# Performance work log

Hardware: AMD Instinct MI355X
Metric: run time of the kernel (lower is better)

Reference implementation:

```python
import jax, jax.numpy as jnp
import numpy as np

B, S, E, H = 2, 2048, 1024, 16
D = E // H  # dim per head


def setup_inputs() -> dict:
    key = jax.random.key(0)
    ks = jax.random.split(key, 13)
    sc = 1.0 / np.sqrt(E)
    inp = {
        "query": jax.random.normal(ks[0], (B, S, E), jnp.float32),
        "key": jax.random.normal(ks[1], (B, S, E), jnp.float32),
        "value": jax.random.normal(ks[2], (B, S, E), jnp.float32),
        "mask": jax.random.randint(ks[3], (B, S, S), 0, 2, jnp.int32),
        "Wq": jax.random.normal(ks[4], (E, E), jnp.float32) * sc,
        "bq": jnp.zeros((E,), jnp.float32),
        "Wk": jax.random.normal(ks[5], (E, E), jnp.float32) * sc,
        "bk": jnp.zeros((E,), jnp.float32),
        "Wv": jax.random.normal(ks[6], (E, E), jnp.float32) * sc,
        "bv": jnp.zeros((E,), jnp.float32),
        "Wo": jax.random.normal(ks[7], (E, E), jnp.float32) * sc,
        "bo": jnp.zeros((E,), jnp.float32),
    }
    return inp


def _split_heads(x):
    # [B, S, E] -> [B, H, S, D]
    return x.reshape(B, S, H, D).transpose(0, 2, 1, 3)


def reference(query, key, value, mask, Wq, bq, Wk, bk, Wv, bv, Wo, bo):
    q = _split_heads(query @ Wq.T + bq)
    k = _split_heads(key @ Wk.T + bk)
    v = _split_heads(value @ Wv.T + bv)

    dk = k.shape[-1]
    # scores: [B, H, Sq, Sk]
    scores = jnp.einsum("bhqd,bhkd->bhqk", q / jnp.sqrt(jnp.asarray(dk, q.dtype)), k)
    # mask broadcast over heads: [B, 1, Sq, Sk]; masked positions get -1e9
    scores = jnp.where(mask[:, None, :, :] == 0, jnp.asarray(-1e9, scores.dtype), scores)
    # fp32 softmax (dropout is identity in eval mode)
    attn = jax.nn.softmax(scores.astype(jnp.float32), axis=-1).astype(q.dtype)
    out = jnp.einsum("bhqk,bhkd->bhqd", attn, v)
    out = out.transpose(0, 2, 1, 3).reshape(B, S, E)
    return out @ Wo.T + bo
```

## Files before the change

kernel.cpp:

```cpp
#include <hip/hip_runtime.h>
#include <hip/hip_bf16.h>
#include <stdint.h>


typedef __bf16 bf16x8 __attribute__((ext_vector_type(8)));
typedef __bf16 bf16x4 __attribute__((ext_vector_type(4)));
typedef float  f32x4  __attribute__((ext_vector_type(4)));
typedef unsigned int u32x4 __attribute__((ext_vector_type(4)));

#define MFMA16(a, b, c) __builtin_amdgcn_mfma_f32_16x16x32_bf16((a), (b), (c), 0, 0, 0)

#if __has_builtin(__builtin_amdgcn_exp2f)
#define EXP2(x) __builtin_amdgcn_exp2f(x)
#else
#define EXP2(x) exp2f(x)
#endif

static constexpr int kB = 2, kS = 2048, kE = 1024, kH = 16, kD = 64;
static constexpr int kM = kB * kS;
static constexpr int kMaskWordsPerRow = kS / 64;
static constexpr float kLog2e = 1.4426950408889634f;

__device__ __forceinline__ void gload_lds16(const void* g, void* l) {
  __builtin_amdgcn_global_load_lds(
      (const __attribute__((address_space(1))) unsigned int*)g,
      (__attribute__((address_space(3))) unsigned int*)l, 16, 0, 0);
}

__device__ __forceinline__ unsigned pack_bf16x2(float a, float b) {
  unsigned short lo = __builtin_bit_cast(unsigned short, (__bf16)a);
  unsigned short hi = __builtin_bit_cast(unsigned short, (__bf16)b);
  return (unsigned)lo | ((unsigned)hi << 16);
}

__global__ __launch_bounds__(256) void cvt_pack_kernel(
    const float* __restrict__ q, const float* __restrict__ k, const float* __restrict__ v,
    const float* __restrict__ wq, const float* __restrict__ wk,
    const float* __restrict__ wv, const float* __restrict__ wo,
    const int* __restrict__ mask,
    __bf16* __restrict__ qb, __bf16* __restrict__ kb, __bf16* __restrict__ vb,
    __bf16* __restrict__ wqb, __bf16* __restrict__ wkb,
    __bf16* __restrict__ wvb, __bf16* __restrict__ wob,
    unsigned long long* __restrict__ mw) {
  const int z = blockIdx.y;
  if (z == 7) {
    const int lane = threadIdx.x & 63;
    const int wid = (blockIdx.x * blockDim.x + threadIdx.x) >> 6;
    const int nwaves = (gridDim.x * blockDim.x) >> 6;
    const int nwords = kB * kS * kMaskWordsPerRow;
    for (int w = wid; w < nwords; w += nwaves) {
      int mv = mask[(size_t)w * 64 + lane];
      unsigned long long bits = __ballot(mv != 0);
      if (lane == 0) mw[w] = bits;
    }
    return;
  }
  const float* src; __bf16* dst; int n;
  switch (z) {
    case 0: src = q;  dst = qb;  n = kM * kE; break;
    case 1: src = k;  dst = kb;  n = kM * kE; break;
    case 2: src = v;  dst = vb;  n = kM * kE; break;
    case 3: src = wq; dst = wqb; n = kE * kE; break;
    case 4: src = wk; dst = wkb; n = kE * kE; break;
    case 5: src = wv; dst = wvb; n = kE * kE; break;
    default: src = wo; dst = wob; n = kE * kE; break;
  }
  const int n4 = n >> 2;
  const int stride = gridDim.x * blockDim.x;
  for (int i = blockIdx.x * blockDim.x + threadIdx.x; i < n4; i += stride) {
    float4 f = ((const float4*)src)[i];
    bf16x4 o = {(__bf16)f.x, (__bf16)f.y, (__bf16)f.z, (__bf16)f.w};
    ((bf16x4*)dst)[i] = o;
  }
}

__global__ __launch_bounds__(256) void gemm_bt(
    const __bf16* __restrict__ A0, const __bf16* __restrict__ A1, const __bf16* __restrict__ A2,
    const __bf16* __restrict__ W0, const __bf16* __restrict__ W1, const __bf16* __restrict__ W2,
    const float* __restrict__ b0, const float* __restrict__ b1, const float* __restrict__ b2,
    __bf16* __restrict__ O0, __bf16* __restrict__ O1, __bf16* __restrict__ O2) {
  const int z = blockIdx.z;
  const __bf16* A = (z == 0) ? A0 : (z == 1) ? A1 : A2;
  const __bf16* W = (z == 0) ? W0 : (z == 1) ? W1 : W2;
  const float* bias = (z == 0) ? b0 : (z == 1) ? b1 : b2;
  __bf16* OutB = (z == 0) ? O0 : (z == 1) ? O1 : O2;
  const float scale = (z == 0) ? 0.125f * kLog2e : 1.0f;

  const int n0 = blockIdx.x * 128;
  const int m0 = blockIdx.y * 128;
  const int tid = threadIdx.x;
  const int wave = tid >> 6, lane = tid & 63;
  const int g = lane >> 4, qi = lane & 15;
  const int wm = wave >> 1, wn = wave & 1;

  __shared__ __align__(16) __bf16 As[128 * 32];
  __shared__ __align__(16) __bf16 Bs[128 * 32];
  __shared__ __align__(16) __bf16 Ts[64 * 136];

  f32x4 acc[4][4];
#pragma unroll
  for (int i = 0; i < 4; ++i)
#pragma unroll
    for (int jj = 0; jj < 4; ++jj) acc[i][jj] = (f32x4){0.f, 0.f, 0.f, 0.f};

  for (int k0 = 0; k0 < kE; k0 += 32) {
#pragma unroll
    for (int jj = 0; jj < 2; ++jj) {
      const int c = jj * 256 + tid;
      const int r = c >> 2, sl = c & 3;
      gload_lds16(&A[(size_t)(m0 + r) * kE + k0 + sl * 8], &As[c * 8]);
      gload_lds16(&W[(size_t)(n0 + r) * kE + k0 + sl * 8], &Bs[c * 8]);
    }
    __syncthreads();

    bf16x8 af[4], bfr[4];
#pragma unroll
    for (int mi = 0; mi < 4; ++mi)
      af[mi] = *(const bf16x8*)&As[(wm * 64 + mi * 16 + qi) * 32 + g * 8];
#pragma unroll
    for (int nj = 0; nj < 4; ++nj)
      bfr[nj] = *(const bf16x8*)&Bs[(wn * 64 + nj * 16 + qi) * 32 + g * 8];
#pragma unroll
    for (int mi = 0; mi < 4; ++mi)
#pragma unroll
      for (int nj = 0; nj < 4; ++nj)
        acc[mi][nj] = MFMA16(af[mi], bfr[nj], acc[mi][nj]);
    __syncthreads();
  }

  if (z == 2) {
    const int bb = m0 >> 11, ss0 = m0 & 2047;
#pragma unroll
    for (int half = 0; half < 2; ++half) {
      __syncthreads();
      if (wn == half) {
#pragma unroll
        for (int nj = 0; nj < 4; ++nj) {
          const int dl = nj * 16 + qi;
          const float bn = bias[n0 + half * 64 + dl];
#pragma unroll
          for (int mi = 0; mi < 4; ++mi) {
            const int srow = wm * 64 + mi * 16 + g * 4;
            bf16x4 o;
#pragma unroll
            for (int r = 0; r < 4; ++r) o[r] = (__bf16)(acc[mi][nj][r] + bn);
            *(bf16x4*)&Ts[dl * 136 + srow] = o;
          }
        }
      }
      __syncthreads();
      const int drow = tid >> 2, sc = (tid & 3) * 32;
      const int head = (n0 + half * 64) >> 6;
      __bf16* dst = OutB + (((size_t)bb * kH + head) * kD + drow) * kS + ss0 + sc;
#pragma unroll
      for (int jj = 0; jj < 4; ++jj) {
        bf16x8 vv = *(const bf16x8*)&Ts[drow * 136 + sc + jj * 8];
        *(bf16x8*)&dst[jj * 8] = vv;
      }
    }
    return;
  }

#pragma unroll
  for (int nj = 0; nj < 4; ++nj) {
    const int ncol = n0 + wn * 64 + nj * 16 + qi;
    const float bn = bias[ncol];
    const int hh = ncol >> 6, dd = ncol & 63;
#pragma unroll
    for (int mi = 0; mi < 4; ++mi) {
#pragma unroll
      for (int r = 0; r < 4; ++r) {
        const int mrow = m0 + wm * 64 + mi * 16 + g * 4 + r;
        const float vv = (acc[mi][nj][r] + bn) * scale;
        const int bb = mrow >> 11, ss = mrow & 2047;
        OutB[((((size_t)bb * kH + hh) * kS + ss) << 6) + dd] = (__bf16)vv;
      }
    }
  }
}

__global__ __launch_bounds__(256) void gemm_out64(
    const __bf16* __restrict__ A, const __bf16* __restrict__ W,
    const float* __restrict__ bias, float* __restrict__ OF) {
  const int n0 = blockIdx.x * 64;
  const int m0 = blockIdx.y * 128;
  const int tid = threadIdx.x;
  const int wave = tid >> 6, lane = tid & 63;
  const int g = lane >> 4, qi = lane & 15;
  const int wm = wave >> 1, wn = wave & 1;

  __shared__ __align__(16) __bf16 As[128 * 32];
  __shared__ __align__(16) __bf16 Bs[64 * 32];

  f32x4 acc[4][2];
#pragma unroll
  for (int i = 0; i < 4; ++i)
#pragma unroll
    for (int jj = 0; jj < 2; ++jj) acc[i][jj] = (f32x4){0.f, 0.f, 0.f, 0.f};

  for (int k0 = 0; k0 < kE; k0 += 32) {
#pragma unroll
    for (int jj = 0; jj < 2; ++jj) {
      const int c = jj * 256 + tid;
      const int r = c >> 2, sl = c & 3;
      gload_lds16(&A[(size_t)(m0 + r) * kE + k0 + sl * 8], &As[c * 8]);
    }
    {
      const int r = tid >> 2, sl = tid & 3;
      gload_lds16(&W[(size_t)(n0 + r) * kE + k0 + sl * 8], &Bs[tid * 8]);
    }
    __syncthreads();

    bf16x8 af[4], bfr[2];
#pragma unroll
    for (int mi = 0; mi < 4; ++mi)
      af[mi] = *(const bf16x8*)&As[(wm * 64 + mi * 16 + qi) * 32 + g * 8];
#pragma unroll
    for (int nj = 0; nj < 2; ++nj)
      bfr[nj] = *(const bf16x8*)&Bs[(wn * 32 + nj * 16 + qi) * 32 + g * 8];
#pragma unroll
    for (int mi = 0; mi < 4; ++mi)
#pragma unroll
      for (int nj = 0; nj < 2; ++nj)
        acc[mi][nj] = MFMA16(af[mi], bfr[nj], acc[mi][nj]);
    __syncthreads();
  }

#pragma unroll
  for (int nj = 0; nj < 2; ++nj) {
    const int ncol = n0 + wn * 32 + nj * 16 + qi;
    const float bn = bias[ncol];
#pragma unroll
    for (int mi = 0; mi < 4; ++mi)
#pragma unroll
      for (int r = 0; r < 4; ++r) {
        const int mrow = m0 + wm * 64 + mi * 16 + g * 4 + r;
        OF[(size_t)mrow * kE + ncol] = acc[mi][nj][r] + bn;
      }
  }
}

__global__ __launch_bounds__(512, 4) void attn_kernel(
    const __bf16* __restrict__ Qh, const __bf16* __restrict__ Kh,
    const __bf16* __restrict__ Vt, const unsigned long long* __restrict__ mw,
    __bf16* __restrict__ Ob) {
  const int tid = threadIdx.x;
  const int wave = tid >> 6, lane = tid & 63;
  const int g = lane >> 4, qi = lane & 15;
  const int id = blockIdx.x;
  const int xcd = id & 7, j = id >> 3;
  const int bh = xcd * 4 + (j >> 4);
  const int qb = j & 15;
  const int b = bh >> 4, h = bh & 15;

  __shared__ __align__(16) __bf16 Ks[2][64 * 64];
  __shared__ __align__(16) __bf16 Vs[2][64 * 64];

  const __bf16* Qp = Qh + (size_t)bh * kS * kD;
  const __bf16* Kp = Kh + (size_t)bh * kS * kD;
  const __bf16* Vp = Vt + (size_t)bh * kD * kS;

  const int q0 = qb * 128 + wave * 16 + qi;
  const unsigned long long* M0 = mw + (size_t)(b * kS + q0) * kMaskWordsPerRow;

  const bf16x8 qf0 = *(const bf16x8*)&Qp[(size_t)q0 * kD + g * 8];
  const bf16x8 qf1 = *(const bf16x8*)&Qp[(size_t)q0 * kD + 32 + g * 8];

  f32x4 acc[4];
#pragma unroll
  for (int f = 0; f < 4; ++f) acc[f] = (f32x4){0.f, 0.f, 0.f, 0.f};
  float den = 0.f;
  const float ninf = __builtin_bit_cast(float, 0xff800000u);

  const int srow = tid >> 3, ssl = tid & 7;
  const int ssls = ssl ^ (srow & 7);
  auto stage = [&](int buf, int kv0) {
    gload_lds16(&Kp[(size_t)(kv0 + srow) * kD + ssls * 8], &Ks[buf][tid * 8]);
    gload_lds16(&Vp[(size_t)srow * kS + kv0 + ssls * 8], &Vs[buf][tid * 8]);
  };

  stage(0, 0);
  __syncthreads();

  const int sw = qi & 7;
  for (int t = 0; t < 32; ++t) {
    const int cur = t & 1;
    if (t < 31) stage(cur ^ 1, (t + 1) * 64);
    const unsigned long long w = M0[t];
    const unsigned wlo = (unsigned)(w >> (g * 4));
    const unsigned whi = (unsigned)(w >> (32 + g * 4));
    const unsigned wf[4] = {wlo, wlo >> 16, whi, whi >> 16};

    float p[16];
    __builtin_amdgcn_s_setprio(1);
#pragma unroll
    for (int f = 0; f < 4; ++f) {
      const int r = f * 16 + qi;
      const bf16x8 k0 = *(const bf16x8*)&Ks[cur][r * 64 + ((g ^ sw) * 8)];
      const bf16x8 k1 = *(const bf16x8*)&Ks[cur][r * 64 + (((4 + g) ^ sw) * 8)];
      f32x4 st = (f32x4){0.f, 0.f, 0.f, 0.f};
      st = MFMA16(k0, qf0, st);
      st = MFMA16(k1, qf1, st);
#pragma unroll
      for (int r4 = 0; r4 < 4; ++r4)
        p[4 * f + r4] = (wf[f] & (1u << r4)) ? st[r4] : ninf;
    }
    __builtin_amdgcn_s_setprio(0);

#pragma unroll
    for (int i = 0; i < 16; ++i) {
      p[i] = EXP2(p[i]);
      den += p[i];
    }

    unsigned pk[4][2];
#pragma unroll
    for (int f = 0; f < 4; ++f) {
      pk[f][0] = pack_bf16x2(p[4 * f + 0], p[4 * f + 1]);
      pk[f][1] = pack_bf16x2(p[4 * f + 2], p[4 * f + 3]);
    }
#pragma unroll
    for (int c = 0; c < 2; ++c) {
      unsigned bw[4];
#pragma unroll
      for (int t4 = 0; t4 < 4; ++t4) {
        const int src = qi + 16 * ((t4 >> 1) + 2 * (g & 1));
        const int vA = __shfl((int)pk[2 * c + 0][t4 & 1], src);
        const int vB = __shfl((int)pk[2 * c + 1][t4 & 1], src);
        bw[t4] = (g >= 2) ? (unsigned)vB : (unsigned)vA;
      }
      const u32x4 tmp = {bw[0], bw[1], bw[2], bw[3]};
      const bf16x8 pb = __builtin_bit_cast(bf16x8, tmp);
      __builtin_amdgcn_s_setprio(1);
#pragma unroll
      for (int f = 0; f < 4; ++f) {
        const int r = f * 16 + qi;
        const bf16x8 vfr =
            *(const bf16x8*)&Vs[cur][r * 64 + (((c * 4 + g) ^ sw) * 8)];
        acc[f] = MFMA16(vfr, pb, acc[f]);
      }
      __builtin_amdgcn_s_setprio(0);
    }
    __syncthreads();
  }

  den += __shfl_xor(den, 16);
  den += __shfl_xor(den, 32);
  const float rinv = 1.0f / den;
  __bf16* Op = Ob + (size_t)(b * kS + q0) * kE + h * kD;
#pragma unroll
  for (int f = 0; f < 4; ++f) {
    ushort4 o;
    o.x = __builtin_bit_cast(unsigned short, (__bf16)(acc[f][0] * rinv));
    o.y = __builtin_bit_cast(unsigned short, (__bf16)(acc[f][1] * rinv));
    o.z = __builtin_bit_cast(unsigned short, (__bf16)(acc[f][2] * rinv));
    o.w = __builtin_bit_cast(unsigned short, (__bf16)(acc[f][3] * rinv));
    *(ushort4*)&Op[f * 16 + g * 4] = o;
  }
}

extern "C" void kernel_launch(void* const* d_in, const int* in_sizes, int n_in,
                              void* d_out, int out_size, void* d_ws, size_t ws_size,
                              hipStream_t stream) {
  (void)in_sizes; (void)n_in; (void)out_size; (void)ws_size;
  const float* q  = (const float*)d_in[0];
  const float* k  = (const float*)d_in[1];
  const float* v  = (const float*)d_in[2];
  const int*   mask = (const int*)d_in[3];
  const float* Wq = (const float*)d_in[4];
  const float* bq = (const float*)d_in[5];
  const float* Wk = (const float*)d_in[6];
  const float* bk = (const float*)d_in[7];
  const float* Wv = (const float*)d_in[8];
  const float* bv = (const float*)d_in[9];
  const float* Wo = (const float*)d_in[10];
  const float* bo = (const float*)d_in[11];

  char* ws = (char*)d_ws;
  const size_t MB = 1024 * 1024;
  __bf16* qb  = (__bf16*)(ws + 0 * MB);
  __bf16* kb  = (__bf16*)(ws + 8 * MB);
  __bf16* vb  = (__bf16*)(ws + 16 * MB);
  __bf16* wqb = (__bf16*)(ws + 24 * MB);
  __bf16* wkb = (__bf16*)(ws + 26 * MB);
  __bf16* wvb = (__bf16*)(ws + 28 * MB);
  __bf16* wob = (__bf16*)(ws + 30 * MB);
  __bf16* Qh  = (__bf16*)(ws + 32 * MB);
  __bf16* Kh  = (__bf16*)(ws + 40 * MB);
  __bf16* Vt  = (__bf16*)(ws + 48 * MB);
  unsigned long long* mwords = (unsigned long long*)(ws + 56 * MB);
  __bf16* Ob = qb;

  cvt_pack_kernel<<<dim3(256, 8), 256, 0, stream>>>(
      q, k, v, Wq, Wk, Wv, Wo, mask, qb, kb, vb, wqb, wkb, wvb, wob, mwords);
  gemm_bt<<<dim3(8, 32, 3), 256, 0, stream>>>(qb, kb, vb, wqb, wkb, wvb,
                                              bq, bk, bv, Qh, Kh, Vt);
  attn_kernel<<<512, 512, 0, stream>>>(Qh, Kh, Vt, mwords, Ob);
  gemm_out64<<<dim3(16, 32), 256, 0, stream>>>(Ob, wob, bo, (float*)d_out);
}
```

Before: 328.2 us.

## Double attention KV tile to 128 and rebalance the convert/mask-pack kernel

The attention kernel now stages 128 keys and values per iteration instead of 64, and processes them as two 64-wide sub-steps. This halves the loop trip count and the number of block barriers. The cost is doubled LDS per block (64 KB), which lowers the number of resident blocks per CU. The convert kernel moves to a 1D grid with block counts assigned per tensor, converts 8 floats per thread, and packs 4 mask words per wave iteration to balance the memory-bound work better.

```diff
diff --git a/kernel.cpp b/kernel.cpp
--- a/kernel.cpp
+++ b/kernel.cpp
@@ -32,6 +32,8 @@
   unsigned short hi = __builtin_bit_cast(unsigned short, (__bf16)b);
   return (unsigned)lo | ((unsigned)hi << 16);
 }
+
+static constexpr int kCvtBlocks = 1664;
 
 __global__ __launch_bounds__(256) void cvt_pack_kernel(
     const float* __restrict__ q, const float* __restrict__ k, const float* __restrict__ v,
@@ -42,35 +44,51 @@
     __bf16* __restrict__ wqb, __bf16* __restrict__ wkb,
     __bf16* __restrict__ wvb, __bf16* __restrict__ wob,
     unsigned long long* __restrict__ mw) {
-  const int z = blockIdx.y;
-  if (z == 7) {
-    const int lane = threadIdx.x & 63;
-    const int wid = (blockIdx.x * blockDim.x + threadIdx.x) >> 6;
-    const int nwaves = (gridDim.x * blockDim.x) >> 6;
-    const int nwords = kB * kS * kMaskWordsPerRow;
-    for (int w = wid; w < nwords; w += nwaves) {
-      int mv = mask[(size_t)w * 64 + lane];
-      unsigned long long bits = __ballot(mv != 0);
-      if (lane == 0) mw[w] = bits;
+  const int bid = blockIdx.x;
+  if (bid < 1216) {
+    const float* src; __bf16* dst; int n8, t0, stride;
+    if (bid < 960) {
+      const int seg = bid / 320, sb = bid - seg * 320;
+      src = (seg == 0) ? q : (seg == 1) ? k : v;
+      dst = (seg == 0) ? qb : (seg == 1) ? kb : vb;
+      n8 = (kM * kE) >> 3;
+      t0 = sb * 256 + threadIdx.x;
+      stride = 320 * 256;
+    } else {
+      const int wseg = (bid - 960) >> 6, sb = (bid - 960) & 63;
+      src = (wseg == 0) ? wq : (wseg == 1) ? wk : (wseg == 2) ? wv : wo;
+      dst = (wseg == 0) ? wqb : (wseg == 1) ? wkb : (wseg == 2) ? wvb : wob;
+      n8 = (kE * kE) >> 3;
+      t0 = sb * 256 + threadIdx.x;
+      stride = 64 * 256;
+    }
+    for (int i = t0; i < n8; i += stride) {
+      float4 f0 = ((const float4*)src)[2 * i];
+      float4 f1 = ((const float4*)src)[2 * i + 1];
+      bf16x8 o = {(__bf16)f0.x, (__bf16)f0.y, (__bf16)f0.z, (__bf16)f0.w,
+                  (__bf16)f1.x, (__bf16)f1.y, (__bf16)f1.z, (__bf16)f1.w};
+      ((bf16x8*)dst)[i] = o;
     }
     return;
   }
-  const float* src; __bf16* dst; int n;
-  switch (z) {
-    case 0: src = q;  dst = qb;  n = kM * kE; break;
-    case 1: src = k;  dst = kb;  n = kM * kE; break;
-    case 2: src = v;  dst = vb;  n = kM * kE; break;
-    case 3: src = wq; dst = wqb; n = kE * kE; break;
-    case 4: src = wk; dst = wkb; n = kE * kE; break;
-    case 5: src = wv; dst = wvb; n = kE * kE; break;
-    default: src = wo; dst = wob; n = kE * kE; break;
-  }
-  const int n4 = n >> 2;
-  const int stride = gridDim.x * blockDim.x;
-  for (int i = blockIdx.x * blockDim.x + threadIdx.x; i < n4; i += stride) {
-    float4 f = ((const float4*)src)[i];
-    bf16x4 o = {(__bf16)f.x, (__bf16)f.y, (__bf16)f.z, (__bf16)f.w};
-    ((bf16x4*)dst)[i] = o;
+  const int lane = threadIdx.x & 63;
+  const int wid = ((bid - 1216) * 4 + (threadIdx.x >> 6));
+  const int nwords = kB * kS * kMaskWordsPerRow;
+  const int stride4 = 1792 * 4;
+  for (int w = wid * 4; w < nwords; w += stride4) {
+    const int v0 = mask[(size_t)(w + 0) * 64 + lane];
+    const int v1 = mask[(size_t)(w + 1) * 64 + lane];
+    const int v2 = mask[(size_t)(w + 2) * 64 + lane];
+    const int v3 = mask[(size_t)(w + 3) * 64 + lane];
+    const unsigned long long b0 = __ballot(v0 != 0);
+    const unsigned long long b1 = __ballot(v1 != 0);
+    const unsigned long long b2 = __ballot(v2 != 0);
+    const unsigned long long b3 = __ballot(v3 != 0);
+    if (lane == 0) {
+      ulonglong2 lo = {b0, b1}, hi = {b2, b3};
+      *(ulonglong2*)&mw[w] = lo;
+      *(ulonglong2*)&mw[w + 2] = hi;
+    }
   }
 }
 
@@ -253,8 +271,8 @@
   const int qb = j & 15;
   const int b = bh >> 4, h = bh & 15;
 
-  __shared__ __align__(16) __bf16 Ks[2][64 * 64];
-  __shared__ __align__(16) __bf16 Vs[2][64 * 64];
+  __shared__ __align__(16) __bf16 Ks[2][128 * 64];
+  __shared__ __align__(16) __bf16 Vs[2][64 * 128];
 
   const __bf16* Qp = Qh + (size_t)bh * kS * kD;
   const __bf16* Kp = Kh + (size_t)bh * kS * kD;
@@ -272,74 +290,84 @@
   float den = 0.f;
   const float ninf = __builtin_bit_cast(float, 0xff800000u);
 
-  const int srow = tid >> 3, ssl = tid & 7;
-  const int ssls = ssl ^ (srow & 7);
   auto stage = [&](int buf, int kv0) {
-    gload_lds16(&Kp[(size_t)(kv0 + srow) * kD + ssls * 8], &Ks[buf][tid * 8]);
-    gload_lds16(&Vp[(size_t)srow * kS + kv0 + ssls * 8], &Vs[buf][tid * 8]);
+#pragma unroll
+    for (int jj = 0; jj < 2; ++jj) {
+      const int c = jj * 512 + tid;
+      const int kr = c >> 3, ksl = c & 7;
+      gload_lds16(&Kp[(size_t)(kv0 + kr) * kD + (ksl ^ (kr & 7)) * 8],
+                  &Ks[buf][c * 8]);
+      const int vr = c >> 4, vsl = c & 15;
+      gload_lds16(&Vp[(size_t)vr * kS + kv0 + (vsl ^ (vr & 7)) * 8],
+                  &Vs[buf][c * 8]);
+    }
   };
 
   stage(0, 0);
   __syncthreads();
 
   const int sw = qi & 7;
-  for (int t = 0; t < 32; ++t) {
+  for (int t = 0; t < 16; ++t) {
     const int cur = t & 1;
-    if (t < 31) stage(cur ^ 1, (t + 1) * 64);
-    const unsigned long long w = M0[t];
-    const unsigned wlo = (unsigned)(w >> (g * 4));
-    const unsigned whi = (unsigned)(w >> (32 + g * 4));
-    const unsigned wf[4] = {wlo, wlo >> 16, whi, whi >> 16};
-
-    float p[16];
-    __builtin_amdgcn_s_setprio(1);
-#pragma unroll
-    for (int f = 0; f < 4; ++f) {
-      const int r = f * 16 + qi;
-      const bf16x8 k0 = *(const bf16x8*)&Ks[cur][r * 64 + ((g ^ sw) * 8)];
-      const bf16x8 k1 = *(const bf16x8*)&Ks[cur][r * 64 + (((4 + g) ^ sw) * 8)];
-      f32x4 st = (f32x4){0.f, 0.f, 0.f, 0.f};
-      st = MFMA16(k0, qf0, st);
-      st = MFMA16(k1, qf1, st);
-#pragma unroll
-      for (int r4 = 0; r4 < 4; ++r4)
-        p[4 * f + r4] = (wf[f] & (1u << r4)) ? st[r4] : ninf;
-    }
-    __builtin_amdgcn_s_setprio(0);
-
-#pragma unroll
-    for (int i = 0; i < 16; ++i) {
-      p[i] = EXP2(p[i]);
-      den += p[i];
-    }
-
-    unsigned pk[4][2];
-#pragma unroll
-    for (int f = 0; f < 4; ++f) {
-      pk[f][0] = pack_bf16x2(p[4 * f + 0], p[4 * f + 1]);
-      pk[f][1] = pack_bf16x2(p[4 * f + 2], p[4 * f + 3]);
-    }
-#pragma unroll
-    for (int c = 0; c < 2; ++c) {
-      unsigned bw[4];
-#pragma unroll
-      for (int t4 = 0; t4 < 4; ++t4) {
-        const int src = qi + 16 * ((t4 >> 1) + 2 * (g & 1));
-        const int vA = __shfl((int)pk[2 * c + 0][t4 & 1], src);
-        const int vB = __shfl((int)pk[2 * c + 1][t4 & 1], src);
-        bw[t4] = (g >= 2) ? (unsigned)vB : (unsigned)vA;
-      }
-      const u32x4 tmp = {bw[0], bw[1], bw[2], bw[3]};
-      const bf16x8 pb = __builtin_bit_cast(bf16x8, tmp);
+    if (t < 15) stage(cur ^ 1, (t + 1) * 128);
+    const ulonglong2 wpair = *(const ulonglong2*)&M0[2 * t];
+#pragma unroll
+    for (int u = 0; u < 2; ++u) {
+      const unsigned long long w = u ? wpair.y : wpair.x;
+      const unsigned wlo = (unsigned)(w >> (g * 4));
+      const unsigned whi = (unsigned)(w >> (32 + g * 4));
+      const unsigned wf[4] = {wlo, wlo >> 16, whi, whi >> 16};
+
+      float p[16];
       __builtin_amdgcn_s_setprio(1);
 #pragma unroll
       for (int f = 0; f < 4; ++f) {
-        const int r = f * 16 + qi;
-        const bf16x8 vfr =
-            *(const bf16x8*)&Vs[cur][r * 64 + (((c * 4 + g) ^ sw) * 8)];
-        acc[f] = MFMA16(vfr, pb, acc[f]);
+        const int r = u * 64 + f * 16 + qi;
+        const bf16x8 k0 = *(const bf16x8*)&Ks[cur][r * 64 + ((g ^ sw) * 8)];
+        const bf16x8 k1 = *(const bf16x8*)&Ks[cur][r * 64 + (((4 + g) ^ sw) * 8)];
+        f32x4 st = (f32x4){0.f, 0.f, 0.f, 0.f};
+        st = MFMA16(k0, qf0, st);
+        st = MFMA16(k1, qf1, st);
+#pragma unroll
+        for (int r4 = 0; r4 < 4; ++r4)
+          p[4 * f + r4] = (wf[f] & (1u << r4)) ? st[r4] : ninf;
       }
       __builtin_amdgcn_s_setprio(0);
+
+#pragma unroll
+      for (int i = 0; i < 16; ++i) {
+        p[i] = EXP2(p[i]);
+        den += p[i];
+      }
+
+      unsigned pk[4][2];
+#pragma unroll
+      for (int f = 0; f < 4; ++f) {
+        pk[f][0] = pack_bf16x2(p[4 * f + 0], p[4 * f + 1]);
+        pk[f][1] = pack_bf16x2(p[4 * f + 2], p[4 * f + 3]);
+      }
+#pragma unroll
+      for (int c = 0; c < 2; ++c) {
+        unsigned bw[4];
+#pragma unroll
+        for (int t4 = 0; t4 < 4; ++t4) {
+          const int src = qi + 16 * ((t4 >> 1) + 2 * (g & 1));
+          const int vA = __shfl((int)pk[2 * c + 0][t4 & 1], src);
+          const int vB = __shfl((int)pk[2 * c + 1][t4 & 1], src);
+          bw[t4] = (g >= 2) ? (unsigned)vB : (unsigned)vA;
+        }
+        const u32x4 tmp = {bw[0], bw[1], bw[2], bw[3]};
+        const bf16x8 pb = __builtin_bit_cast(bf16x8, tmp);
+        __builtin_amdgcn_s_setprio(1);
+#pragma unroll
+        for (int f = 0; f < 4; ++f) {
+          const int rd = f * 16 + qi;
+          const int slot = (u * 8 + c * 4 + g) ^ sw;
+          const bf16x8 vfr = *(const bf16x8*)&Vs[cur][rd * 128 + slot * 8];
+          acc[f] = MFMA16(vfr, pb, acc[f]);
+        }
+        __builtin_amdgcn_s_setprio(0);
+      }
     }
     __syncthreads();
   }
@@ -391,7 +419,7 @@
   unsigned long long* mwords = (unsigned long long*)(ws + 56 * MB);
   __bf16* Ob = qb;
 
-  cvt_pack_kernel<<<dim3(256, 8), 256, 0, stream>>>(
+  cvt_pack_kernel<<<kCvtBlocks, 256, 0, stream>>>(
       q, k, v, Wq, Wk, Wv, Wo, mask, qb, kb, vb, wqb, wkb, wvb, wob, mwords);
   gemm_bt<<<dim3(8, 32, 3), 256, 0, stream>>>(qb, kb, vb, wqb, wkb, wvb,
                                               bq, bk, bv, Qh, Kh, Vt);
```

Result: faster. 285.9 us (-12.9%).
